# Performance work log

Hardware: AMD Instinct MI355X
Metric: run time of the kernel (lower is better)

## Reference

```python
import jax, jax.numpy as jnp
import numpy as np
from jax import lax

# dimension numbers for a true 4D convolution: layout is (N, C, s1, s2, s3, s4)
_DN = lax.ConvDimensionNumbers(lhs_spec=(0, 1, 2, 3, 4, 5),
                               rhs_spec=(0, 1, 2, 3, 4, 5),
                               out_spec=(0, 1, 2, 3, 4, 5))


def _conv4d(x, w, b):
    # x: [B, Cin, H1, W1, H2, W2], w: [Cout, Cin, 3, 3, 3, 3], 'same' padding
    y = lax.conv_general_dilated(x, w, window_strides=(1, 1, 1, 1),
                                 padding='SAME', dimension_numbers=_DN)
    return y + b.reshape(1, -1, 1, 1, 1, 1)


def _ncnet(x, W1, b1, W2, b2, W3, b3):
    h = jax.nn.relu(_conv4d(x, W1, b1))
    h = jax.nn.relu(_conv4d(h, W2, b2))
    h = jax.nn.relu(_conv4d(h, W3, b3))
    return h


def setup_inputs() -> dict:
    key = jax.random.key(0)
    ks = jax.random.split(key, 7)
    B, G = 4, 32  # batch, grid size (H1=W1=H2=W2=G)
    x = jax.random.normal(ks[0], (B, 1, G, G, G, G), dtype=jnp.float32)
    s1 = 1.0 / np.sqrt(1 * 3 ** 4)
    s2 = 1.0 / np.sqrt(10 * 3 ** 4)
    W1 = jax.random.normal(ks[1], (10, 1, 3, 3, 3, 3), dtype=jnp.float32) * s1
    b1 = jax.random.normal(ks[2], (10,), dtype=jnp.float32) * s1
    W2 = jax.random.normal(ks[3], (10, 10, 3, 3, 3, 3), dtype=jnp.float32) * s2
    b2 = jax.random.normal(ks[4], (10,), dtype=jnp.float32) * s2
    W3 = jax.random.normal(ks[5], (1, 10, 3, 3, 3, 3), dtype=jnp.float32) * s2
    b3 = jax.random.normal(ks[6], (1,), dtype=jnp.float32) * s2
    return {"x": x, "W1": W1, "b1": b1, "W2": W2, "b2": b2,
            "W3": W3, "b3": b3}


def reference(x, W1, b1, W2, b2, W3, b3):
    # symmetric mode: f(x) + swap(f(swap(x))) where swap exchanges (H1,W1)<->(H2,W2)
    out_a = _ncnet(x, W1, b1, W2, b2, W3, b3)
    xt = jnp.transpose(x, (0, 1, 4, 5, 2, 3))
    out_b = jnp.transpose(_ncnet(xt, W1, b1, W2, b2, W3, b3),
                          (0, 1, 4, 5, 2, 3))
    return out_a + out_b
```

## Files before the change

kernel.cpp:

```cpp
#include <hip/hip_runtime.h>

#define GSZ 32
#define NPTS (1<<20)

#define XB_FLOATS ((size_t)34*34*34*16)
#define XT ((size_t)34*34*34*32*8)

#define OFF_XB  ((size_t)0)
#define OFF_X2  (XB_FLOATS)
#define BSLOT   (XB_FLOATS + 4*XT)

#define WSB_FLOATS 20480
#define NHALO 6536

typedef __attribute__((ext_vector_type(8)))  short bf16x8;
typedef __attribute__((ext_vector_type(16))) float f32x16;

__device__ __forceinline__ unsigned short f2bf(float f) {
    union { float f; unsigned u; } v; v.f = f;
    unsigned r = v.u + 0x7FFFu + ((v.u >> 16) & 1u);
    return (unsigned short)(r >> 16);
}

__global__ void k_bpack2(const float* __restrict__ W2, unsigned* __restrict__ wsB) {
    int t = threadIdx.x;
    int lane = t & 63, j = t >> 6;
    int n = lane & 31, kh = lane >> 5;
    for (int br = 0; br < 2; ++br)
        for (int g = 0; g < 27; ++g) {
            int d1 = g / 9, d2 = (g / 3) % 3, d3 = g % 3;
            unsigned v = 0;
            for (int e = 0; e < 2; ++e) {
                int k = kh * 8 + 2 * j + e;
                unsigned short h = 0;
                if (k < 10 && n < 30) {
                    int co = n % 10, d4 = n / 10;
                    int tap = br == 0 ? ((d1 * 3 + d2) * 3 + d3) * 3 + d4
                                      : ((d3 * 3 + d4) * 3 + d1) * 3 + d2;
                    h = f2bf(W2[(co * 10 + k) * 81 + tap]);
                }
                v |= (unsigned)h << (16 * e);
            }
            wsB[((br * 27 + g) * 64 + lane) * 4 + j] = v;
        }
}

__global__ void k_bpack3(const float* __restrict__ W3, unsigned* __restrict__ wsB3) {
    int t = threadIdx.x;
    int lane = t & 63, j = t >> 6;
    int n = lane & 31, kh = lane >> 5;
    for (int br = 0; br < 2; ++br)
        for (int g = 0; g < 9; ++g) {
            int d1 = g / 3, d2 = g % 3;
            unsigned v = 0;
            for (int e = 0; e < 2; ++e) {
                int k = kh * 8 + 2 * j + e;
                unsigned short h = 0;
                if (k < 10 && n < 9) {
                    int d3 = n / 3, d4 = n % 3;
                    int tap = br == 0 ? ((d1 * 3 + d2) * 3 + d3) * 3 + d4
                                      : ((d3 * 3 + d4) * 3 + d1) * 3 + d2;
                    h = f2bf(W3[k * 81 + tap]);
                }
                v |= (unsigned)h << (16 * e);
            }
            wsB3[((br * 9 + g) * 64 + lane) * 4 + j] = v;
        }
}

__global__ void k_bpack1(const float* __restrict__ W1, unsigned* __restrict__ wsB1) {
    int t = threadIdx.x;
    int lane = t & 63, jj = t >> 6;
    int n = lane & 31, kh = lane >> 5;
    for (int br = 0; br < 2; ++br)
        for (int g = 0; g < 3; ++g) {
            unsigned v = 0;
            for (int e = 0; e < 2; ++e) {
                int kap = kh * 8 + 2 * jj + e;
                unsigned short h = 0;
                if (kap < 9 && n < 30) {
                    int co = n % 10, d4 = n / 10;
                    int d1 = kap / 3, d2 = kap % 3;
                    int tap = br == 0 ? ((d1 * 3 + d2) * 3 + g) * 3 + d4
                                      : ((g * 3 + d4) * 3 + d1) * 3 + d2;
                    h = f2bf(W1[co * 81 + tap]);
                }
                v |= (unsigned)h << (16 * e);
            }
            wsB1[((br * 3 + g) * 64 + lane) * 4 + jj] = v;
        }
}

__global__ __launch_bounds__(256) void k_zero_halo(float* __restrict__ ws) {
    int wid = blockIdx.x * 4 + (threadIdx.x >> 6);
    if (wid >= NHALO) return;
    int lane = threadIdx.x & 63;
    int i, j, k;
    if (wid < 2312) {
        i = (wid < 1156) ? 0 : 33;
        int r = wid % 1156; j = r / 34; k = r % 34;
    } else if (wid < 4488) {
        int r = wid - 2312;
        i = 1 + r / 68;
        int r2 = r % 68;
        j = (r2 < 34) ? 0 : 33;
        k = r2 % 34;
    } else {
        int r = wid - 4488;
        i = 1 + r / 64;
        int r2 = r % 64;
        j = 1 + (r2 >> 1);
        k = (r2 & 1) ? 33 : 0;
    }
    size_t line = (size_t)(i * 34 + j) * 34 + k;
    float* slot = ws + (size_t)blockIdx.y * BSLOT;
    uint4 z4 = make_uint4(0u, 0u, 0u, 0u);
#pragma unroll
    for (int tns = 0; tns < 4; ++tns)
        ((uint4*)(slot + OFF_X2 + tns * XT))[line * 64 + lane] = z4;
    if (lane < 4) ((uint4*)(slot + OFF_XB))[line * 4 + lane] = z4;
}

__global__ __launch_bounds__(256) void k_copy_in(const float* __restrict__ x,
                                                 float* __restrict__ ws, int b0) {
    int b = b0 + blockIdx.z;
    int gid = blockIdx.x * 256 + threadIdx.x;
    int l = gid & 31, k = (gid >> 5) & 31, j = (gid >> 10) & 31, i = gid >> 15;
    float v = x[(size_t)b * NPTS + gid];
    unsigned short* XB = (unsigned short*)(ws + (size_t)blockIdx.z * BSLOT + OFF_XB);
    XB[((size_t)(((i + 1) * 34 + (j + 1)) * 34 + (k + 1))) * 32 + l] = f2bf(v);
}

__global__ __launch_bounds__(256) void k_conv1m(const unsigned* __restrict__ wsB1,
                                                const float* __restrict__ B1,
                                                float* ws) {
    __shared__ float epi[4][34 * 33];
    int t = threadIdx.x, lane = t & 63, wv = t >> 6;
    int zb = blockIdx.z >> 2, br = (blockIdx.z >> 1) & 1, w = blockIdx.z & 1;
    int bid = blockIdx.x;
    int s = ((bid & 7) << 7) | (bid >> 3);
    int i = s >> 5, j = s & 31;
    int k0g = w * 16 + wv * 4;
    int q = lane & 31, half = lane >> 5;

    float bias[8];
#pragma unroll
    for (int e = 0; e < 8; ++e) {
        int co = half * 8 + e;
        bias[e] = (co < 10) ? B1[co] : 0.f;
    }
    if (lane < 33) { epi[wv][lane] = 0.f; epi[wv][33 * 33 + lane] = 0.f; }

    float* slot = ws + (size_t)zb * BSLOT;
    const unsigned short* XB = (const unsigned short*)(slot + OFF_XB);
    const unsigned short* xb = XB + ((size_t)((i * 34 + j) * 34 + k0g)) * 32 + q;
    const bf16x8* Bg = (const bf16x8*)(wsB1 + br * 3 * 64 * 4);

    bf16x8 A[6];
    if (half == 0) {
#pragma unroll
        for (int kk = 0; kk < 6; ++kk) {
            bf16x8 a;
#pragma unroll
            for (int e = 0; e < 8; ++e) {
                const int d1 = e / 3, d2 = e % 3;
                a[e] = (short)xb[(size_t)(d1 * 34 + d2) * 1088 + kk * 32];
            }
            A[kk] = a;
        }
    } else {
#pragma unroll
        for (int kk = 0; kk < 6; ++kk) {
            bf16x8 a = {};
            a[0] = (short)xb[(size_t)(2 * 34 + 2) * 1088 + kk * 32];
            A[kk] = a;
        }
    }
    bf16x8 Bf[3];
#pragma unroll
    for (int d3 = 0; d3 < 3; ++d3) Bf[d3] = Bg[d3 * 64 + lane];

    f32x16 D[4] = {};
#pragma unroll
    for (int kk = 0; kk < 6; ++kk)
#pragma unroll
        for (int m = 0; m < 4; ++m) {
            int d3 = kk - m;
            if (d3 >= 0 && d3 < 3)
                D[m] = __builtin_amdgcn_mfma_f32_32x32x16_bf16(A[kk], Bf[d3], D[m], 0, 0, 0);
        }

    float* epw = epi[wv];
    unsigned short* X2 = (unsigned short*)(slot + OFF_X2 + (size_t)br * XT);
#pragma unroll
    for (int m = 0; m < 4; ++m) {
#pragma unroll
        for (int r = 0; r < 16; ++r) {
            int row = (r & 3) + 8 * (r >> 2) + 4 * half;
            epw[(row + 1) * 33 + q] = D[m][r];
        }
        unsigned u[4];
#pragma unroll
        for (int e = 0; e < 4; ++e) {
            unsigned short h2[2];
#pragma unroll
            for (int xx = 0; xx < 2; ++xx) {
                int co = half * 8 + 2 * e + xx;
                float v = 0.f;
                if (co < 10) {
                    v = bias[2 * e + xx];
#pragma unroll
                    for (int ss = 0; ss < 3; ++ss)
                        v += epw[(q + ss) * 33 + ss * 10 + co];
                    v = fmaxf(v, 0.f);
                }
                h2[xx] = f2bf(v);
            }
            u[e] = (unsigned)h2[0] | ((unsigned)h2[1] << 16);
        }
        unsigned short* dst = X2 + ((size_t)(((i + 1) * 34 + (j + 1)) * 34 + (k0g + m + 1))) * 512
                              + q * 16 + half * 8;
        *(uint4*)dst = make_uint4(u[0], u[1], u[2], u[3]);
    }
}

__global__ __launch_bounds__(256) void k_conv2m(const unsigned* __restrict__ wsB,
                                                const float* __restrict__ B2,
                                                float* ws) {
    __shared__ float epi[4][34 * 33];

    int t = threadIdx.x;
    int lane = t & 63, wv = t >> 6;
    int zb = blockIdx.z >> 2, br = (blockIdx.z >> 1) & 1, w = blockIdx.z & 1;
    int bid = blockIdx.x;
    int s = ((bid & 7) << 7) | (bid >> 3);
    int i = s >> 5, j = s & 31;
    int k0 = (w * 4 + wv) * 4;

    if (lane < 33) { epi[wv][lane] = 0.f; epi[wv][33 * 33 + lane] = 0.f; }

    int q = lane & 31, half = lane >> 5;
    float bias[8];
#pragma unroll
    for (int e = 0; e < 8; ++e) {
        int co = half * 8 + e;
        bias[e] = (co < 10) ? B2[co] : 0.f;
    }

    float* slot = ws + (size_t)zb * BSLOT;
    const unsigned short* X2 = (const unsigned short*)(slot + OFF_X2 + (size_t)br * XT);
    const unsigned short* base0 = X2 + ((size_t)((i * 34 + j) * 34 + k0)) * 512
                                  + q * 16 + half * 8;
    const bf16x8* Bg = (const bf16x8*)(wsB + br * 27 * 64 * 4);

    f32x16 D[4] = {};

#pragma unroll 1
    for (int d1 = 0; d1 < 3; ++d1)
#pragma unroll 1
        for (int d2 = 0; d2 < 3; ++d2) {
            int g = d1 * 3 + d2;
            const unsigned short* pg = base0 + (size_t)(d1 * 1156 + d2 * 34) * 512;
            bf16x8 A[6];
#pragma unroll
            for (int kk = 0; kk < 6; ++kk)
                A[kk] = *(const bf16x8*)(pg + kk * 512);
            bf16x8 Bf[3];
#pragma unroll
            for (int d3 = 0; d3 < 3; ++d3)
                Bf[d3] = Bg[(g * 3 + d3) * 64 + lane];
#pragma unroll
            for (int kk = 0; kk < 6; ++kk)
#pragma unroll
                for (int m = 0; m < 4; ++m) {
                    int d3 = kk - m;
                    if (d3 >= 0 && d3 < 3)
                        D[m] = __builtin_amdgcn_mfma_f32_32x32x16_bf16(A[kk], Bf[d3], D[m], 0, 0, 0);
                }
        }

    float* epw = epi[wv];
    unsigned short* X3 = (unsigned short*)(slot + OFF_X2 + (size_t)(2 + br) * XT);
#pragma unroll
    for (int m = 0; m < 4; ++m) {
#pragma unroll
        for (int r = 0; r < 16; ++r) {
            int row = (r & 3) + 8 * (r >> 2) + 4 * half;
            epw[(row + 1) * 33 + q] = D[m][r];
        }
        unsigned u[4];
#pragma unroll
        for (int e = 0; e < 4; ++e) {
            unsigned short h2[2];
#pragma unroll
            for (int xx = 0; xx < 2; ++xx) {
                int co = half * 8 + 2 * e + xx;
                float v = 0.f;
                if (co < 10) {
                    v = bias[2 * e + xx];
#pragma unroll
                    for (int ss = 0; ss < 3; ++ss)
                        v += epw[(q + ss) * 33 + ss * 10 + co];
                    v = fmaxf(v, 0.f);
                }
                h2[xx] = f2bf(v);
            }
            u[e] = (unsigned)h2[0] | ((unsigned)h2[1] << 16);
        }
        unsigned short* dst = X3 + ((size_t)(((i + 1) * 34 + (j + 1)) * 34 + (k0 + m + 1))) * 512
                              + q * 16 + half * 8;
        *(uint4*)dst = make_uint4(u[0], u[1], u[2], u[3]);
    }
}

__global__ __launch_bounds__(256) void k_conv3m(const unsigned* __restrict__ wsB3,
                                                const float* __restrict__ B3,
                                                float* ws, float* __restrict__ out,
                                                int b0, int br) {
    __shared__ float epi[4][6 * 34 * 9];

    int t = threadIdx.x;
    int lane = t & 63, wv = t >> 6;
    int zb = blockIdx.z >> 1, w = blockIdx.z & 1;
    int b = b0 + zb;
    int bid = blockIdx.x;
    int s = ((bid & 7) << 7) | (bid >> 3);
    int i = s >> 5, j = s & 31;
    int k0 = (w * 4 + wv) * 4;

    for (int idx = lane; idx < 6 * 9; idx += 64) {
        int rel = idx / 9, c = idx % 9;
        epi[wv][(rel * 34 + 0) * 9 + c] = 0.f;
        epi[wv][(rel * 34 + 33) * 9 + c] = 0.f;
    }

    float* slot = ws + (size_t)zb * BSLOT;
    const unsigned short* X3 = (const unsigned short*)(slot + OFF_X2 + (size_t)(2 + br) * XT);
    const unsigned short* base0 = X3 + ((size_t)((i * 34 + j) * 34 + k0)) * 512
                                  + (lane & 31) * 16 + (lane >> 5) * 8;
    const bf16x8* Bg = (const bf16x8*)(wsB3 + br * 9 * 64 * 4);

    f32x16 D[6] = {};

#pragma unroll 1
    for (int g = 0; g < 9; ++g) {
        const unsigned short* pg = base0 + (size_t)((g / 3) * 1156 + (g % 3) * 34) * 512;
        bf16x8 Bf = Bg[g * 64 + lane];
#pragma unroll
        for (int rel = 0; rel < 6; ++rel) {
            bf16x8 A = *(const bf16x8*)(pg + rel * 512);
            D[rel] = __builtin_amdgcn_mfma_f32_32x32x16_bf16(A, Bf, D[rel], 0, 0, 0);
        }
    }

    int q = lane & 31, half = lane >> 5;
    float* epw = epi[wv];
    if (q < 9) {
#pragma unroll
        for (int rel = 0; rel < 6; ++rel)
#pragma unroll
            for (int r = 0; r < 16; ++r) {
                int row = (r & 3) + 8 * (r >> 2) + 4 * half;
                epw[(rel * 34 + row + 1) * 9 + q] = D[rel][r];
            }
    }
    float bb = B3[0];
    float vout[4];
#pragma unroll
    for (int m = 0; m < 4; ++m) {
        float v = bb;
#pragma unroll
        for (int d3 = 0; d3 < 3; ++d3)
#pragma unroll
            for (int d4 = 0; d4 < 3; ++d4)
                v += epw[((m + d3) * 34 + (q + d4)) * 9 + d3 * 3 + d4];
        vout[m] = fmaxf(v, 0.f);
    }

    float* dst = out + (size_t)b * NPTS;
    if (half == 0) {
        if (br == 0) {
#pragma unroll
            for (int m = 0; m < 4; ++m)
                dst[(size_t)i * 32768 + j * 1024 + (k0 + m) * 32 + q] = vout[m];
        } else {
#pragma unroll
            for (int m = 0; m < 4; ++m) {
                size_t o = (size_t)i * 32768 + j * 1024 + (k0 + m) * 32 + q;
                dst[o] = dst[o] + vout[m];
            }
        }
    }
}

extern "C" void kernel_launch(void* const* d_in, const int* in_sizes, int n_in,
                              void* d_out, int out_size, void* d_ws, size_t ws_size,
                              hipStream_t stream) {
    const float* x  = (const float*)d_in[0];
    const float* W1 = (const float*)d_in[1];
    const float* b1 = (const float*)d_in[2];
    const float* W2 = (const float*)d_in[3];
    const float* b2 = (const float*)d_in[4];
    const float* W3 = (const float*)d_in[5];
    const float* b3 = (const float*)d_in[6];
    float* out = (float*)d_out;
    float* ws  = (float*)d_ws;
    float* slots = ws + WSB_FLOATS;
    unsigned* wsB2 = (unsigned*)ws;
    unsigned* wsB3 = (unsigned*)ws + 13824;
    unsigned* wsB1 = (unsigned*)ws + 18432;

    size_t slot_bytes = BSLOT * sizeof(float);
    int GB = (int)((ws_size - WSB_FLOATS * 4) / slot_bytes);
    if (GB > 2) GB = 2;
    if (GB < 1) GB = 1;

    k_zero_halo<<<dim3((NHALO + 3) / 4, GB), 256, 0, stream>>>(slots);
    k_bpack2<<<1, 256, 0, stream>>>(W2, wsB2);
    k_bpack3<<<1, 256, 0, stream>>>(W3, wsB3);
    k_bpack1<<<1, 256, 0, stream>>>(W1, wsB1);

    for (int b0 = 0; b0 < 4; b0 += GB) {
        int gb = 4 - b0 < GB ? 4 - b0 : GB;
        k_copy_in<<<dim3(4096, 1, gb), 256, 0, stream>>>(x, slots, b0);
        k_conv1m<<<dim3(1024, 1, 4 * gb), 256, 0, stream>>>(wsB1, b1, slots);
        k_conv2m<<<dim3(1024, 1, 4 * gb), 256, 0, stream>>>(wsB2, b2, slots);
        k_conv3m<<<dim3(1024, 1, 2 * gb), 256, 0, stream>>>(wsB3, b3, slots, out, b0, 0);
        k_conv3m<<<dim3(1024, 1, 2 * gb), 256, 0, stream>>>(wsB3, b3, slots, out, b0, 1);
    }
}
```

Baseline: 651.2 us.

## Merge weight packing, vectorize copy-in, fuse conv3 branches, narrow padded-K loads

Combines the three weight-packing kernels into one launch. Vectorizes the input copy with float4 loads and ushort4 stores. Fuses both symmetric branches of conv3 into one kernel so the output is written once instead of read-modify-written. In conv2 and conv3, the upper half-wave, whose K slots hold only channels 8-9 plus zero padding, now loads a single dword and zero-fills the rest, cutting global load bytes at the cost of divergent code paths.

```diff
diff --git a/kernel.cpp b/kernel.cpp
--- a/kernel.cpp
+++ b/kernel.cpp
@@ -22,7 +22,10 @@
     return (unsigned short)(r >> 16);
 }
 
-__global__ void k_bpack2(const float* __restrict__ W2, unsigned* __restrict__ wsB) {
+__global__ void k_bpack_all(const float* __restrict__ W1, const float* __restrict__ W2,
+                            const float* __restrict__ W3,
+                            unsigned* __restrict__ wsB2, unsigned* __restrict__ wsB3,
+                            unsigned* __restrict__ wsB1) {
     int t = threadIdx.x;
     int lane = t & 63, j = t >> 6;
     int n = lane & 31, kh = lane >> 5;
@@ -41,14 +44,8 @@
                 }
                 v |= (unsigned)h << (16 * e);
             }
-            wsB[((br * 27 + g) * 64 + lane) * 4 + j] = v;
-        }
-}
-
-__global__ void k_bpack3(const float* __restrict__ W3, unsigned* __restrict__ wsB3) {
-    int t = threadIdx.x;
-    int lane = t & 63, j = t >> 6;
-    int n = lane & 31, kh = lane >> 5;
+            wsB2[((br * 27 + g) * 64 + lane) * 4 + j] = v;
+        }
     for (int br = 0; br < 2; ++br)
         for (int g = 0; g < 9; ++g) {
             int d1 = g / 3, d2 = g % 3;
@@ -66,17 +63,11 @@
             }
             wsB3[((br * 9 + g) * 64 + lane) * 4 + j] = v;
         }
-}
-
-__global__ void k_bpack1(const float* __restrict__ W1, unsigned* __restrict__ wsB1) {
-    int t = threadIdx.x;
-    int lane = t & 63, jj = t >> 6;
-    int n = lane & 31, kh = lane >> 5;
     for (int br = 0; br < 2; ++br)
         for (int g = 0; g < 3; ++g) {
             unsigned v = 0;
             for (int e = 0; e < 2; ++e) {
-                int kap = kh * 8 + 2 * jj + e;
+                int kap = kh * 8 + 2 * j + e;
                 unsigned short h = 0;
                 if (kap < 9 && n < 30) {
                     int co = n % 10, d4 = n / 10;
@@ -87,7 +78,7 @@
                 }
                 v |= (unsigned)h << (16 * e);
             }
-            wsB1[((br * 3 + g) * 64 + lane) * 4 + jj] = v;
+            wsB1[((br * 3 + g) * 64 + lane) * 4 + j] = v;
         }
 }
 
@@ -125,10 +116,13 @@
                                                  float* __restrict__ ws, int b0) {
     int b = b0 + blockIdx.z;
     int gid = blockIdx.x * 256 + threadIdx.x;
-    int l = gid & 31, k = (gid >> 5) & 31, j = (gid >> 10) & 31, i = gid >> 15;
-    float v = x[(size_t)b * NPTS + gid];
+    int l0 = (gid & 7) * 4;
+    int k = (gid >> 3) & 31, j = (gid >> 8) & 31, i = gid >> 13;
+    float4 v = *(const float4*)(x + (size_t)b * NPTS + (size_t)gid * 4);
+    ushort4 h;
+    h.x = f2bf(v.x); h.y = f2bf(v.y); h.z = f2bf(v.z); h.w = f2bf(v.w);
     unsigned short* XB = (unsigned short*)(ws + (size_t)blockIdx.z * BSLOT + OFF_XB);
-    XB[((size_t)(((i + 1) * 34 + (j + 1)) * 34 + (k + 1))) * 32 + l] = f2bf(v);
+    *(ushort4*)(XB + ((size_t)(((i + 1) * 34 + (j + 1)) * 34 + (k + 1))) * 32 + l0) = h;
 }
 
 __global__ __launch_bounds__(256) void k_conv1m(const unsigned* __restrict__ wsB1,
@@ -262,13 +256,32 @@
             int g = d1 * 3 + d2;
             const unsigned short* pg = base0 + (size_t)(d1 * 1156 + d2 * 34) * 512;
             bf16x8 A[6];
-#pragma unroll
-            for (int kk = 0; kk < 6; ++kk)
-                A[kk] = *(const bf16x8*)(pg + kk * 512);
             bf16x8 Bf[3];
-#pragma unroll
-            for (int d3 = 0; d3 < 3; ++d3)
-                Bf[d3] = Bg[(g * 3 + d3) * 64 + lane];
+            if (half == 0) {
+#pragma unroll
+                for (int kk = 0; kk < 6; ++kk)
+                    A[kk] = *(const bf16x8*)(pg + kk * 512);
+#pragma unroll
+                for (int d3 = 0; d3 < 3; ++d3)
+                    Bf[d3] = Bg[(g * 3 + d3) * 64 + lane];
+            } else {
+#pragma unroll
+                for (int kk = 0; kk < 6; ++kk) {
+                    unsigned d = *(const unsigned*)(pg + kk * 512);
+                    bf16x8 a = {};
+                    a[0] = (short)(d & 0xffffu);
+                    a[1] = (short)(d >> 16);
+                    A[kk] = a;
+                }
+#pragma unroll
+                for (int d3 = 0; d3 < 3; ++d3) {
+                    unsigned d = *(const unsigned*)(Bg + (g * 3 + d3) * 64 + lane);
+                    bf16x8 b = {};
+                    b[0] = (short)(d & 0xffffu);
+                    b[1] = (short)(d >> 16);
+                    Bf[d3] = b;
+                }
+            }
 #pragma unroll
             for (int kk = 0; kk < 6; ++kk)
 #pragma unroll
@@ -316,7 +329,7 @@
 __global__ __launch_bounds__(256) void k_conv3m(const unsigned* __restrict__ wsB3,
                                                 const float* __restrict__ B3,
                                                 float* ws, float* __restrict__ out,
-                                                int b0, int br) {
+                                                int b0) {
     __shared__ float epi[4][6 * 34 * 9];
 
     int t = threadIdx.x;
@@ -327,6 +340,7 @@
     int s = ((bid & 7) << 7) | (bid >> 3);
     int i = s >> 5, j = s & 31;
     int k0 = (w * 4 + wv) * 4;
+    int q = lane & 31, half = lane >> 5;
 
     for (int idx = lane; idx < 6 * 9; idx += 64) {
         int rel = idx / 9, c = idx % 9;
@@ -335,62 +349,76 @@
     }
 
     float* slot = ws + (size_t)zb * BSLOT;
-    const unsigned short* X3 = (const unsigned short*)(slot + OFF_X2 + (size_t)(2 + br) * XT);
-    const unsigned short* base0 = X3 + ((size_t)((i * 34 + j) * 34 + k0)) * 512
-                                  + (lane & 31) * 16 + (lane >> 5) * 8;
-    const bf16x8* Bg = (const bf16x8*)(wsB3 + br * 9 * 64 * 4);
-
-    f32x16 D[6] = {};
+    float* epw = epi[wv];
+    float bb = B3[0];
+    float vsum[4];
 
 #pragma unroll 1
-    for (int g = 0; g < 9; ++g) {
-        const unsigned short* pg = base0 + (size_t)((g / 3) * 1156 + (g % 3) * 34) * 512;
-        bf16x8 Bf = Bg[g * 64 + lane];
-#pragma unroll
-        for (int rel = 0; rel < 6; ++rel) {
-            bf16x8 A = *(const bf16x8*)(pg + rel * 512);
-            D[rel] = __builtin_amdgcn_mfma_f32_32x32x16_bf16(A, Bf, D[rel], 0, 0, 0);
-        }
-    }
-
-    int q = lane & 31, half = lane >> 5;
-    float* epw = epi[wv];
-    if (q < 9) {
-#pragma unroll
-        for (int rel = 0; rel < 6; ++rel)
-#pragma unroll
-            for (int r = 0; r < 16; ++r) {
-                int row = (r & 3) + 8 * (r >> 2) + 4 * half;
-                epw[(rel * 34 + row + 1) * 9 + q] = D[rel][r];
-            }
-    }
-    float bb = B3[0];
-    float vout[4];
-#pragma unroll
-    for (int m = 0; m < 4; ++m) {
-        float v = bb;
-#pragma unroll
-        for (int d3 = 0; d3 < 3; ++d3)
-#pragma unroll
-            for (int d4 = 0; d4 < 3; ++d4)
-                v += epw[((m + d3) * 34 + (q + d4)) * 9 + d3 * 3 + d4];
-        vout[m] = fmaxf(v, 0.f);
+    for (int br = 0; br < 2; ++br) {
+        const unsigned short* X3 = (const unsigned short*)(slot + OFF_X2 + (size_t)(2 + br) * XT);
+        const unsigned short* base0 = X3 + ((size_t)((i * 34 + j) * 34 + k0)) * 512
+                                      + q * 16 + half * 8;
+        const bf16x8* Bg = (const bf16x8*)(wsB3 + br * 9 * 64 * 4);
+
+        f32x16 D[6] = {};
+
+#pragma unroll 1
+        for (int g = 0; g < 9; ++g) {
+            const unsigned short* pg = base0 + (size_t)((g / 3) * 1156 + (g % 3) * 34) * 512;
+            bf16x8 A6[6];
+            bf16x8 Bf;
+            if (half == 0) {
+#pragma unroll
+                for (int rel = 0; rel < 6; ++rel)
+                    A6[rel] = *(const bf16x8*)(pg + rel * 512);
+                Bf = Bg[g * 64 + lane];
+            } else {
+#pragma unroll
+                for (int rel = 0; rel < 6; ++rel) {
+                    unsigned d = *(const unsigned*)(pg + rel * 512);
+                    bf16x8 a = {};
+                    a[0] = (short)(d & 0xffffu);
+                    a[1] = (short)(d >> 16);
+                    A6[rel] = a;
+                }
+                unsigned d = *(const unsigned*)(Bg + g * 64 + lane);
+                bf16x8 bt = {};
+                bt[0] = (short)(d & 0xffffu);
+                bt[1] = (short)(d >> 16);
+                Bf = bt;
+            }
+#pragma unroll
+            for (int rel = 0; rel < 6; ++rel)
+                D[rel] = __builtin_amdgcn_mfma_f32_32x32x16_bf16(A6[rel], Bf, D[rel], 0, 0, 0);
+        }
+
+        if (q < 9) {
+#pragma unroll
+            for (int rel = 0; rel < 6; ++rel)
+#pragma unroll
+                for (int r = 0; r < 16; ++r) {
+                    int row = (r & 3) + 8 * (r >> 2) + 4 * half;
+                    epw[(rel * 34 + row + 1) * 9 + q] = D[rel][r];
+                }
+        }
+#pragma unroll
+        for (int m = 0; m < 4; ++m) {
+            float v = bb;
+#pragma unroll
+            for (int d3 = 0; d3 < 3; ++d3)
+#pragma unroll
+                for (int d4 = 0; d4 < 3; ++d4)
+                    v += epw[((m + d3) * 34 + (q + d4)) * 9 + d3 * 3 + d4];
+            v = fmaxf(v, 0.f);
+            if (br == 0) vsum[m] = v; else vsum[m] += v;
+        }
     }
 
     float* dst = out + (size_t)b * NPTS;
-    if (half == 0) {
-        if (br == 0) {
-#pragma unroll
-            for (int m = 0; m < 4; ++m)
-                dst[(size_t)i * 32768 + j * 1024 + (k0 + m) * 32 + q] = vout[m];
-        } else {
-#pragma unroll
-            for (int m = 0; m < 4; ++m) {
-                size_t o = (size_t)i * 32768 + j * 1024 + (k0 + m) * 32 + q;
-                dst[o] = dst[o] + vout[m];
-            }
-        }
-    }
+    if (half == 0)
+#pragma unroll
+        for (int m = 0; m < 4; ++m)
+            dst[(size_t)i * 32768 + j * 1024 + (k0 + m) * 32 + q] = vsum[m];
 }
 
 extern "C" void kernel_launch(void* const* d_in, const int* in_sizes, int n_in,
@@ -416,16 +444,13 @@
     if (GB < 1) GB = 1;
 
     k_zero_halo<<<dim3((NHALO + 3) / 4, GB), 256, 0, stream>>>(slots);
-    k_bpack2<<<1, 256, 0, stream>>>(W2, wsB2);
-    k_bpack3<<<1, 256, 0, stream>>>(W3, wsB3);
-    k_bpack1<<<1, 256, 0, stream>>>(W1, wsB1);
+    k_bpack_all<<<1, 256, 0, stream>>>(W1, W2, W3, wsB2, wsB3, wsB1);
 
     for (int b0 = 0; b0 < 4; b0 += GB) {
         int gb = 4 - b0 < GB ? 4 - b0 : GB;
-        k_copy_in<<<dim3(4096, 1, gb), 256, 0, stream>>>(x, slots, b0);
+        k_copy_in<<<dim3(1024, 1, gb), 256, 0, stream>>>(x, slots, b0);
         k_conv1m<<<dim3(1024, 1, 4 * gb), 256, 0, stream>>>(wsB1, b1, slots);
         k_conv2m<<<dim3(1024, 1, 4 * gb), 256, 0, stream>>>(wsB2, b2, slots);
-        k_conv3m<<<dim3(1024, 1, 2 * gb), 256, 0, stream>>>(wsB3, b3, slots, out, b0, 0);
-        k_conv3m<<<dim3(1024, 1, 2 * gb), 256, 0, stream>>>(wsB3, b3, slots, out, b0, 1);
-    }
-}
+        k_conv3m<<<dim3(1024, 1, 2 * gb), 256, 0, stream>>>(wsB3, b3, slots, out, b0);
+    }
+}
```

After: 945.8 us. 45.2% more time.
